# Performance work log

Measured on AMD Instinct MI355X. Metric: run time of the kernel, lower is better.

## Reference

```python
import jax, jax.numpy as jnp
import numpy as np

B, T, I, H = 256, 512, 128, 256


def setup_inputs() -> dict:
    key = jax.random.key(0)
    ks = jax.random.split(key, 12)
    xav = lambda k, shape: jax.random.normal(k, shape, jnp.float32) * jnp.sqrt(2.0 / (shape[0] + shape[1]))
    return {
        'x': jax.random.normal(ks[0], (B, T, I), jnp.float32),
        'weight_xr': xav(ks[1], (H, I)), 'weight_hr': xav(ks[2], (H, H)), 'bias_r': jnp.zeros((H,), jnp.float32),
        'weight_xz': xav(ks[3], (H, I)), 'weight_hz': xav(ks[4], (H, H)), 'bias_z': jnp.zeros((H,), jnp.float32),
        'weight_x': xav(ks[5], (H, I)), 'weight_h': xav(ks[6], (H, H)), 'bias': jnp.zeros((H,), jnp.float32),
        'w1': xav(ks[7], (64, H)), 'b1': jnp.zeros((64,), jnp.float32),
        'w2': xav(ks[8], (10, 64)), 'b2': jnp.zeros((10,), jnp.float32),
    }


def _gru_final(x, weight_xr, weight_hr, bias_r, weight_xz, weight_hz, bias_z,
               weight_x, weight_h, bias):
    # Precompute input projections for all timesteps: [B,T,H] each
    xr = jnp.einsum('bti,hi->bth', x, weight_xr) + bias_r
    xz = jnp.einsum('bti,hi->bth', x, weight_xz) + bias_z
    xn = jnp.einsum('bti,hi->bth', x, weight_x) + bias

    def step(h, inp):
        xr_t, xz_t, xn_t = inp  # each [B,H]
        r = jax.nn.sigmoid(xr_t + h @ weight_hr.T)
        z = jax.nn.sigmoid(xz_t + h @ weight_hz.T)
        ht = jnp.tanh(xn_t + (r * h) @ weight_h.T)
        h_new = z * h + (1.0 - z) * ht
        return h_new, None

    h0 = jnp.zeros((x.shape[0], weight_hr.shape[0]), x.dtype)
    # scan over time: inputs [T,B,H]
    h_final, _ = jax.lax.scan(step, h0, (xr.transpose(1, 0, 2), xz.transpose(1, 0, 2), xn.transpose(1, 0, 2)))
    return h_final


def reference(x, weight_xr, weight_hr, bias_r, weight_xz, weight_hz, bias_z,
              weight_x, weight_h, bias, w1, b1, w2, b2):
    h = _gru_final(x, weight_xr, weight_hr, bias_r, weight_xz, weight_hz, bias_z,
                   weight_x, weight_h, bias)
    h = jax.nn.sigmoid(h)
    h = jax.nn.sigmoid(h @ w1.T + b1)
    return jax.nn.softmax(h @ w2.T + b2, axis=1)
```

## Files before the change

### kernel.cpp

```cpp
#include <hip/hip_runtime.h>


typedef _Float16 half8 __attribute__((ext_vector_type(8)));
typedef float    f32x4 __attribute__((ext_vector_type(4)));

#define BARRIER() asm volatile("s_waitcnt lgkmcnt(0)\n\ts_barrier" ::: "memory")

__device__ __forceinline__ unsigned short f2s(float f) {
    _Float16 h = (_Float16)f; unsigned short s; __builtin_memcpy(&s, &h, 2); return s;
}
__device__ __forceinline__ float s2f(unsigned short s) {
    _Float16 h; __builtin_memcpy(&h, &s, 2); return (float)h;
}
__device__ __forceinline__ float fast_sigmoid(float x) {
    return __builtin_amdgcn_rcpf(1.0f + __builtin_amdgcn_exp2f(-1.4426950408889634f * x));
}
__device__ __forceinline__ float fast_tanh(float x) {
    return 1.0f - 2.0f * __builtin_amdgcn_rcpf(1.0f + __builtin_amdgcn_exp2f(2.885390081777927f * x));
}
__device__ __forceinline__ unsigned int pk2(float lo, float hi) {
    return (unsigned int)f2s(lo) | ((unsigned int)f2s(hi) << 16);
}
__device__ __forceinline__ f32x4 up4(uint2 u) {
    return (f32x4){ s2f((unsigned short)u.x), s2f((unsigned short)(u.x >> 16)),
                    s2f((unsigned short)u.y), s2f((unsigned short)(u.y >> 16)) };
}
union H8U4 { half8 h; uint4 u; };
__device__ __forceinline__ half8 ldg_h8(const unsigned short* p) {
    H8U4 t; t.u = *reinterpret_cast<const uint4*>(p); return t.h;
}
__device__ __forceinline__ half8 pack8(float4 a, float4 b) {
    half8 r;
    r[0] = (_Float16)a.x; r[1] = (_Float16)a.y; r[2] = (_Float16)a.z; r[3] = (_Float16)a.w;
    r[4] = (_Float16)b.x; r[5] = (_Float16)b.y; r[6] = (_Float16)b.z; r[7] = (_Float16)b.w;
    return r;
}

__global__ void pack_w_kernel(const float* __restrict__ whr, const float* __restrict__ whz,
                              const float* __restrict__ wh,  const float* __restrict__ wxr,
                              const float* __restrict__ wxz, const float* __restrict__ wxn,
                              unsigned short* __restrict__ Wall) {
    const int i = blockIdx.x * 256 + threadIdx.x;
    float v;
    if (i < 196608) {
        const int m = i >> 16;
        const int r = i & 65535;
        v = (m == 0 ? whr : (m == 1 ? whz : wh))[r];
    } else {
        const int ii = i - 196608;
        const int m = ii >> 15;
        const int r = ii & 32767;
        v = (m == 0 ? wxr : (m == 1 ? wxz : wxn))[r];
    }
    Wall[i] = f2s(v);
}

__global__ __launch_bounds__(512, 1) void proj_kernel(
    const float* __restrict__ x, const unsigned short* __restrict__ Wxp,
    const float* __restrict__ br, const float* __restrict__ bz, const float* __restrict__ bn,
    unsigned short* __restrict__ P, int t0, int TPB) {
    const int tid = threadIdx.x;
    const int w   = tid >> 6;
    const int lane = tid & 63;
    const int l15 = lane & 15;
    const int lq  = lane >> 4;
    const int btile = blockIdx.x & 15;
    const int tc    = blockIdx.x >> 4;
    const int b0 = btile * 16;

    half8 wf[3][4][2];
#pragma unroll
    for (int g = 0; g < 3; ++g)
#pragma unroll
        for (int kt = 0; kt < 4; ++kt)
#pragma unroll
            for (int ntl = 0; ntl < 2; ++ntl)
                wf[g][kt][ntl] = ldg_h8(Wxp + g * 32768 + (w * 32 + ntl * 16 + l15) * 128 + kt * 32 + 8 * lq);

    const float* bptr[3] = {br, bz, bn};
    float4 bv[3][2];
#pragma unroll
    for (int g = 0; g < 3; ++g)
#pragma unroll
        for (int ntl = 0; ntl < 2; ++ntl)
            bv[g][ntl] = *reinterpret_cast<const float4*>(bptr[g] + (2 * w + ntl) * 16 + 4 * lq);

    for (int i = 0; i < TPB; ++i) {
        const int tl = tc * TPB + i;
        const int t  = t0 + tl;
        half8 xf[4];
#pragma unroll
        for (int kt = 0; kt < 4; ++kt) {
            const float* xp = x + (size_t)(b0 + l15) * 65536 + t * 128 + kt * 32 + 8 * lq;
            float4 f0 = *reinterpret_cast<const float4*>(xp);
            float4 f1 = *reinterpret_cast<const float4*>(xp + 4);
            xf[kt] = pack8(f0, f1);
        }
        unsigned short* Pb = P + (size_t)tl * 196608 + btile * 12288;
#pragma unroll
        for (int g = 0; g < 3; ++g) {
#pragma unroll
            for (int ntl = 0; ntl < 2; ++ntl) {
                f32x4 acc = {0.f, 0.f, 0.f, 0.f};
#pragma unroll
                for (int kt = 0; kt < 4; ++kt)
                    acc = __builtin_amdgcn_mfma_f32_16x16x32_f16(wf[g][kt][ntl], xf[kt], acc, 0, 0, 0);
                uint2 o;
                o.x = pk2(acc[0] + bv[g][ntl].x, acc[1] + bv[g][ntl].y);
                o.y = pk2(acc[2] + bv[g][ntl].z, acc[3] + bv[g][ntl].w);
                *reinterpret_cast<uint2*>(Pb + (2 * w + ntl) * 768 + g * 256 + lane * 4) = o;
            }
        }
    }
}

__global__ __launch_bounds__(512, 1) void rec_kernel(
    const unsigned short* __restrict__ Wp, const unsigned short* __restrict__ P,
    float* __restrict__ h_state, int t0, int Tc) {
    const int tid = threadIdx.x;
    const int w = tid >> 6;
    const int lane = tid & 63;
    const int l15 = lane & 15;
    const int lq = lane >> 4;
    const int btile = blockIdx.x;
    const int b0 = btile * 16;

    __shared__ __align__(16) unsigned short hl[8192];
    char* lds = reinterpret_cast<char*>(hl);

    half8 wr[8][2], wz[8][2], wn[8][2];
#pragma unroll
    for (int kt = 0; kt < 8; ++kt) {
#pragma unroll
        for (int nt = 0; nt < 2; ++nt) {
            const int row = w * 32 + nt * 16 + l15;
            const int co = kt * 32 + 8 * lq;
            wr[kt][nt] = ldg_h8(Wp + row * 256 + co);
            wz[kt][nt] = ldg_h8(Wp + 65536 + row * 256 + co);
            wn[kt][nt] = ldg_h8(Wp + 131072 + row * 256 + co);
        }
    }

    const int b7 = l15 & 7;
    int rdaddr[8];
#pragma unroll
    for (int kt = 0; kt < 8; ++kt)
        rdaddr[kt] = l15 * 512 + (((4 * kt + lq) ^ b7) << 4);
    int waddr[2];
#pragma unroll
    for (int nt = 0; nt < 2; ++nt) {
        const int c = 4 * w + 2 * nt + (lq >> 1);
        waddr[nt] = l15 * 512 + ((c ^ b7) << 4) + 8 * (lq & 1);
    }

    float hreg[2][4];
    if (t0 == 0) {
#pragma unroll
        for (int nt = 0; nt < 2; ++nt)
#pragma unroll
            for (int j = 0; j < 4; ++j) hreg[nt][j] = 0.f;
    } else {
#pragma unroll
        for (int nt = 0; nt < 2; ++nt) {
            float4 v = *reinterpret_cast<const float4*>(
                h_state + (b0 + l15) * 256 + w * 32 + nt * 16 + 4 * lq);
            hreg[nt][0] = v.x; hreg[nt][1] = v.y; hreg[nt][2] = v.z; hreg[nt][3] = v.w;
        }
    }
#pragma unroll
    for (int nt = 0; nt < 2; ++nt) {
        uint2 o;
        o.x = pk2(hreg[nt][0], hreg[nt][1]);
        o.y = pk2(hreg[nt][2], hreg[nt][3]);
        *reinterpret_cast<uint2*>(lds + waddr[nt]) = o;
    }
    BARRIER();

    const unsigned short* Pw = P + btile * 12288 + (2 * w) * 768 + lane * 4;
    uint2 cp[3][2], np[3][2];
#pragma unroll
    for (int g = 0; g < 3; ++g)
#pragma unroll
        for (int nt = 0; nt < 2; ++nt)
            cp[g][nt] = *reinterpret_cast<const uint2*>(Pw + nt * 768 + g * 256);

    for (int tl = 0; tl < Tc; ++tl) {
        const unsigned short* Pn = Pw + (size_t)((tl + 1 < Tc) ? tl + 1 : tl) * 196608;
#pragma unroll
        for (int g = 0; g < 3; ++g)
#pragma unroll
            for (int nt = 0; nt < 2; ++nt)
                np[g][nt] = *reinterpret_cast<const uint2*>(Pn + nt * 768 + g * 256);

        f32x4 aR[2], aZ[2];
        aR[0] = up4(cp[0][0]);
        aR[1] = up4(cp[0][1]);
        aZ[0] = up4(cp[1][0]);
        aZ[1] = up4(cp[1][1]);
#pragma unroll
        for (int kt = 0; kt < 8; ++kt) {
            half8 a = *reinterpret_cast<const half8*>(lds + rdaddr[kt]);
            aR[0] = __builtin_amdgcn_mfma_f32_16x16x32_f16(wr[kt][0], a, aR[0], 0, 0, 0);
            aR[1] = __builtin_amdgcn_mfma_f32_16x16x32_f16(wr[kt][1], a, aR[1], 0, 0, 0);
            aZ[0] = __builtin_amdgcn_mfma_f32_16x16x32_f16(wz[kt][0], a, aZ[0], 0, 0, 0);
            aZ[1] = __builtin_amdgcn_mfma_f32_16x16x32_f16(wz[kt][1], a, aZ[1], 0, 0, 0);
        }
#pragma unroll
        for (int nt = 0; nt < 2; ++nt) {
            const float r0 = fast_sigmoid(aR[nt][0]);
            const float r1 = fast_sigmoid(aR[nt][1]);
            const float r2 = fast_sigmoid(aR[nt][2]);
            const float r3 = fast_sigmoid(aR[nt][3]);
            uint2 o;
            o.x = pk2(r0 * hreg[nt][0], r1 * hreg[nt][1]);
            o.y = pk2(r2 * hreg[nt][2], r3 * hreg[nt][3]);
            *reinterpret_cast<uint2*>(lds + 8192 + waddr[nt]) = o;
        }
        BARRIER();

        float zv[2][4];
#pragma unroll
        for (int nt = 0; nt < 2; ++nt) {
            zv[nt][0] = fast_sigmoid(aZ[nt][0]);
            zv[nt][1] = fast_sigmoid(aZ[nt][1]);
            zv[nt][2] = fast_sigmoid(aZ[nt][2]);
            zv[nt][3] = fast_sigmoid(aZ[nt][3]);
        }
        f32x4 aN[2];
        aN[0] = up4(cp[2][0]);
        aN[1] = up4(cp[2][1]);
#pragma unroll
        for (int kt = 0; kt < 8; ++kt) {
            half8 rf = *reinterpret_cast<const half8*>(lds + 8192 + rdaddr[kt]);
            aN[0] = __builtin_amdgcn_mfma_f32_16x16x32_f16(wn[kt][0], rf, aN[0], 0, 0, 0);
            aN[1] = __builtin_amdgcn_mfma_f32_16x16x32_f16(wn[kt][1], rf, aN[1], 0, 0, 0);
        }
#pragma unroll
        for (int nt = 0; nt < 2; ++nt) {
            const float t0_ = fast_tanh(aN[nt][0]);
            const float t1_ = fast_tanh(aN[nt][1]);
            const float t2_ = fast_tanh(aN[nt][2]);
            const float t3_ = fast_tanh(aN[nt][3]);
            hreg[nt][0] = t0_ + zv[nt][0] * (hreg[nt][0] - t0_);
            hreg[nt][1] = t1_ + zv[nt][1] * (hreg[nt][1] - t1_);
            hreg[nt][2] = t2_ + zv[nt][2] * (hreg[nt][2] - t2_);
            hreg[nt][3] = t3_ + zv[nt][3] * (hreg[nt][3] - t3_);
            uint2 o;
            o.x = pk2(hreg[nt][0], hreg[nt][1]);
            o.y = pk2(hreg[nt][2], hreg[nt][3]);
            *reinterpret_cast<uint2*>(lds + waddr[nt]) = o;
        }
        BARRIER();

#pragma unroll
        for (int g = 0; g < 3; ++g)
#pragma unroll
            for (int nt = 0; nt < 2; ++nt)
                cp[g][nt] = np[g][nt];
    }

#pragma unroll
    for (int nt = 0; nt < 2; ++nt) {
        float4 st;
        st.x = hreg[nt][0]; st.y = hreg[nt][1]; st.z = hreg[nt][2]; st.w = hreg[nt][3];
        *reinterpret_cast<float4*>(h_state + (b0 + l15) * 256 + w * 32 + nt * 16 + 4 * lq) = st;
    }
}

__global__ __launch_bounds__(64) void head_kernel(
    const float* __restrict__ h_state, const float* __restrict__ w1, const float* __restrict__ b1,
    const float* __restrict__ w2, const float* __restrict__ b2, float* __restrict__ out) {
    const int row = blockIdx.x;
    const int lane = threadIdx.x;
    __shared__ float hs[256];
    __shared__ float h2[64];
    __shared__ float lg[10];
    float4 v = *reinterpret_cast<const float4*>(h_state + row * 256 + lane * 4);
    hs[lane * 4 + 0] = fast_sigmoid(v.x);
    hs[lane * 4 + 1] = fast_sigmoid(v.y);
    hs[lane * 4 + 2] = fast_sigmoid(v.z);
    hs[lane * 4 + 3] = fast_sigmoid(v.w);
    __syncthreads();
    float acc = b1[lane];
#pragma unroll 4
    for (int k = 0; k < 256; k += 4) {
        float4 wv = *reinterpret_cast<const float4*>(w1 + lane * 256 + k);
        acc += hs[k] * wv.x + hs[k + 1] * wv.y + hs[k + 2] * wv.z + hs[k + 3] * wv.w;
    }
    h2[lane] = fast_sigmoid(acc);
    __syncthreads();
    if (lane < 10) {
        float a2 = b2[lane];
        for (int k = 0; k < 64; ++k) a2 += h2[k] * w2[lane * 64 + k];
        lg[lane] = a2;
    }
    __syncthreads();
    if (lane < 10) {
        float m = lg[0];
#pragma unroll
        for (int k = 1; k < 10; ++k) m = fmaxf(m, lg[k]);
        float s = 0.f;
#pragma unroll
        for (int k = 0; k < 10; ++k) s += __expf(lg[k] - m);
        out[row * 10 + lane] = __expf(lg[lane] - m) / s;
    }
}

extern "C" void kernel_launch(void* const* d_in, const int* in_sizes, int n_in,
                              void* d_out, int out_size, void* d_ws, size_t ws_size,
                              hipStream_t stream) {
    const float* x   = (const float*)d_in[0];
    const float* wxr = (const float*)d_in[1];
    const float* whr = (const float*)d_in[2];
    const float* br  = (const float*)d_in[3];
    const float* wxz = (const float*)d_in[4];
    const float* whz = (const float*)d_in[5];
    const float* bz  = (const float*)d_in[6];
    const float* wxn = (const float*)d_in[7];
    const float* wh  = (const float*)d_in[8];
    const float* bn  = (const float*)d_in[9];
    const float* w1  = (const float*)d_in[10];
    const float* b1  = (const float*)d_in[11];
    const float* w2  = (const float*)d_in[12];
    const float* b2  = (const float*)d_in[13];
    float* out = (float*)d_out;

    char* ws = (char*)d_ws;
    unsigned short* Wp  = (unsigned short*)ws;
    unsigned short* Wxp = (unsigned short*)(ws + 393216);
    float* h_state = (float*)(ws + 589824);
    unsigned short* P = (unsigned short*)(ws + 851968);
    const size_t avail = (ws_size > 851968) ? ws_size - 851968 : 0;
    int Tc = 512;
    while (Tc > 1 && (size_t)Tc * 393216 > avail) Tc >>= 1;
    const int TPB = Tc < 32 ? Tc : 32;

    pack_w_kernel<<<dim3(1152), 256, 0, stream>>>(whr, whz, wh, wxr, wxz, wxn, Wp);
    for (int t0 = 0; t0 < 512; t0 += Tc) {
        proj_kernel<<<dim3(16 * (Tc / TPB)), 512, 0, stream>>>(x, Wxp, br, bz, bn, P, t0, TPB);
        rec_kernel<<<dim3(16), 512, 0, stream>>>(Wp, P, h_state, t0, Tc);
    }
    head_kernel<<<dim3(256), 64, 0, stream>>>(h_state, w1, b1, w2, b2, out);
}
```

Baseline: 912.6 us.

## Halve recurrence block to 4 waves, each computing 64 hidden columns

The recurrent kernel now launches 256 threads instead of 512, and each wave computes four 16-column tiles of the three gates instead of two. The intent is to cut barrier participants and reuse each LDS read of the hidden state across more MFMAs. In exchange, per-wave register pressure doubles because weights for 64 rows of all three gates are held in registers. There are also fewer waves per SIMD to hide MFMA and transcendental latency on the serial timestep chain.

```diff
diff --git a/kernel.cpp b/kernel.cpp
--- a/kernel.cpp
+++ b/kernel.cpp
@@ -114,7 +114,7 @@
     }
 }
 
-__global__ __launch_bounds__(512, 1) void rec_kernel(
+__global__ __launch_bounds__(256, 1) void rec_kernel(
     const unsigned short* __restrict__ Wp, const unsigned short* __restrict__ P,
     float* __restrict__ h_state, int t0, int Tc) {
     const int tid = threadIdx.x;
@@ -128,16 +128,16 @@
     __shared__ __align__(16) unsigned short hl[8192];
     char* lds = reinterpret_cast<char*>(hl);
 
-    half8 wr[8][2], wz[8][2], wn[8][2];
+    half8 wr[8][4], wz[8][4], wn[8][4];
 #pragma unroll
     for (int kt = 0; kt < 8; ++kt) {
 #pragma unroll
-        for (int nt = 0; nt < 2; ++nt) {
-            const int row = w * 32 + nt * 16 + l15;
+        for (int ntl = 0; ntl < 4; ++ntl) {
+            const int row = w * 64 + ntl * 16 + l15;
             const int co = kt * 32 + 8 * lq;
-            wr[kt][nt] = ldg_h8(Wp + row * 256 + co);
-            wz[kt][nt] = ldg_h8(Wp + 65536 + row * 256 + co);
-            wn[kt][nt] = ldg_h8(Wp + 131072 + row * 256 + co);
+            wr[kt][ntl] = ldg_h8(Wp + row * 256 + co);
+            wz[kt][ntl] = ldg_h8(Wp + 65536 + row * 256 + co);
+            wn[kt][ntl] = ldg_h8(Wp + 131072 + row * 256 + co);
         }
     }
 
@@ -146,124 +146,128 @@
 #pragma unroll
     for (int kt = 0; kt < 8; ++kt)
         rdaddr[kt] = l15 * 512 + (((4 * kt + lq) ^ b7) << 4);
-    int waddr[2];
-#pragma unroll
-    for (int nt = 0; nt < 2; ++nt) {
-        const int c = 4 * w + 2 * nt + (lq >> 1);
-        waddr[nt] = l15 * 512 + ((c ^ b7) << 4) + 8 * (lq & 1);
-    }
-
-    float hreg[2][4];
+    int waddr[4];
+#pragma unroll
+    for (int ntl = 0; ntl < 4; ++ntl) {
+        const int c = 8 * w + 2 * ntl + (lq >> 1);
+        waddr[ntl] = l15 * 512 + ((c ^ b7) << 4) + 8 * (lq & 1);
+    }
+
+    float hreg[4][4];
     if (t0 == 0) {
 #pragma unroll
-        for (int nt = 0; nt < 2; ++nt)
-#pragma unroll
-            for (int j = 0; j < 4; ++j) hreg[nt][j] = 0.f;
+        for (int ntl = 0; ntl < 4; ++ntl)
+#pragma unroll
+            for (int j = 0; j < 4; ++j) hreg[ntl][j] = 0.f;
     } else {
 #pragma unroll
-        for (int nt = 0; nt < 2; ++nt) {
+        for (int ntl = 0; ntl < 4; ++ntl) {
             float4 v = *reinterpret_cast<const float4*>(
-                h_state + (b0 + l15) * 256 + w * 32 + nt * 16 + 4 * lq);
-            hreg[nt][0] = v.x; hreg[nt][1] = v.y; hreg[nt][2] = v.z; hreg[nt][3] = v.w;
-        }
-    }
-#pragma unroll
-    for (int nt = 0; nt < 2; ++nt) {
+                h_state + (b0 + l15) * 256 + w * 64 + ntl * 16 + 4 * lq);
+            hreg[ntl][0] = v.x; hreg[ntl][1] = v.y; hreg[ntl][2] = v.z; hreg[ntl][3] = v.w;
+        }
+    }
+#pragma unroll
+    for (int ntl = 0; ntl < 4; ++ntl) {
         uint2 o;
-        o.x = pk2(hreg[nt][0], hreg[nt][1]);
-        o.y = pk2(hreg[nt][2], hreg[nt][3]);
-        *reinterpret_cast<uint2*>(lds + waddr[nt]) = o;
+        o.x = pk2(hreg[ntl][0], hreg[ntl][1]);
+        o.y = pk2(hreg[ntl][2], hreg[ntl][3]);
+        *reinterpret_cast<uint2*>(lds + waddr[ntl]) = o;
     }
     BARRIER();
 
-    const unsigned short* Pw = P + btile * 12288 + (2 * w) * 768 + lane * 4;
-    uint2 cp[3][2], np[3][2];
+    const unsigned short* Pw = P + btile * 12288 + (4 * w) * 768 + lane * 4;
+    uint2 cp[3][4], np[3][4];
 #pragma unroll
     for (int g = 0; g < 3; ++g)
 #pragma unroll
-        for (int nt = 0; nt < 2; ++nt)
-            cp[g][nt] = *reinterpret_cast<const uint2*>(Pw + nt * 768 + g * 256);
+        for (int ntl = 0; ntl < 4; ++ntl)
+            cp[g][ntl] = *reinterpret_cast<const uint2*>(Pw + ntl * 768 + g * 256);
 
     for (int tl = 0; tl < Tc; ++tl) {
         const unsigned short* Pn = Pw + (size_t)((tl + 1 < Tc) ? tl + 1 : tl) * 196608;
 #pragma unroll
         for (int g = 0; g < 3; ++g)
 #pragma unroll
-            for (int nt = 0; nt < 2; ++nt)
-                np[g][nt] = *reinterpret_cast<const uint2*>(Pn + nt * 768 + g * 256);
-
-        f32x4 aR[2], aZ[2];
-        aR[0] = up4(cp[0][0]);
-        aR[1] = up4(cp[0][1]);
-        aZ[0] = up4(cp[1][0]);
-        aZ[1] = up4(cp[1][1]);
+            for (int ntl = 0; ntl < 4; ++ntl)
+                np[g][ntl] = *reinterpret_cast<const uint2*>(Pn + ntl * 768 + g * 256);
+
+        f32x4 aR[4], aZ[4];
+#pragma unroll
+        for (int ntl = 0; ntl < 4; ++ntl) {
+            aR[ntl] = up4(cp[0][ntl]);
+            aZ[ntl] = up4(cp[1][ntl]);
+        }
 #pragma unroll
         for (int kt = 0; kt < 8; ++kt) {
             half8 a = *reinterpret_cast<const half8*>(lds + rdaddr[kt]);
-            aR[0] = __builtin_amdgcn_mfma_f32_16x16x32_f16(wr[kt][0], a, aR[0], 0, 0, 0);
-            aR[1] = __builtin_amdgcn_mfma_f32_16x16x32_f16(wr[kt][1], a, aR[1], 0, 0, 0);
-            aZ[0] = __builtin_amdgcn_mfma_f32_16x16x32_f16(wz[kt][0], a, aZ[0], 0, 0, 0);
-            aZ[1] = __builtin_amdgcn_mfma_f32_16x16x32_f16(wz[kt][1], a, aZ[1], 0, 0, 0);
-        }
-#pragma unroll
-        for (int nt = 0; nt < 2; ++nt) {
-            const float r0 = fast_sigmoid(aR[nt][0]);
-            const float r1 = fast_sigmoid(aR[nt][1]);
-            const float r2 = fast_sigmoid(aR[nt][2]);
-            const float r3 = fast_sigmoid(aR[nt][3]);
+#pragma unroll
+            for (int ntl = 0; ntl < 4; ++ntl) {
+                aR[ntl] = __builtin_amdgcn_mfma_f32_16x16x32_f16(wr[kt][ntl], a, aR[ntl], 0, 0, 0);
+                aZ[ntl] = __builtin_amdgcn_mfma_f32_16x16x32_f16(wz[kt][ntl], a, aZ[ntl], 0, 0, 0);
+            }
+        }
+#pragma unroll
+        for (int ntl = 0; ntl < 4; ++ntl) {
+            const float r0 = fast_sigmoid(aR[ntl][0]);
+            const float r1 = fast_sigmoid(aR[ntl][1]);
+            const float r2 = fast_sigmoid(aR[ntl][2]);
+            const float r3 = fast_sigmoid(aR[ntl][3]);
             uint2 o;
-            o.x = pk2(r0 * hreg[nt][0], r1 * hreg[nt][1]);
-            o.y = pk2(r2 * hreg[nt][2], r3 * hreg[nt][3]);
-            *reinterpret_cast<uint2*>(lds + 8192 + waddr[nt]) = o;
+            o.x = pk2(r0 * hreg[ntl][0], r1 * hreg[ntl][1]);
+            o.y = pk2(r2 * hreg[ntl][2], r3 * hreg[ntl][3]);
+            *reinterpret_cast<uint2*>(lds + 8192 + waddr[ntl]) = o;
         }
         BARRIER();
 
-        float zv[2][4];
-#pragma unroll
-        for (int nt = 0; nt < 2; ++nt) {
-            zv[nt][0] = fast_sigmoid(aZ[nt][0]);
-            zv[nt][1] = fast_sigmoid(aZ[nt][1]);
-            zv[nt][2] = fast_sigmoid(aZ[nt][2]);
-            zv[nt][3] = fast_sigmoid(aZ[nt][3]);
-        }
-        f32x4 aN[2];
-        aN[0] = up4(cp[2][0]);
-        aN[1] = up4(cp[2][1]);
+        float zv[4][4];
+#pragma unroll
+        for (int ntl = 0; ntl < 4; ++ntl) {
+            zv[ntl][0] = fast_sigmoid(aZ[ntl][0]);
+            zv[ntl][1] = fast_sigmoid(aZ[ntl][1]);
+            zv[ntl][2] = fast_sigmoid(aZ[ntl][2]);
+            zv[ntl][3] = fast_sigmoid(aZ[ntl][3]);
+        }
+        f32x4 aN[4];
+#pragma unroll
+        for (int ntl = 0; ntl < 4; ++ntl)
+            aN[ntl] = up4(cp[2][ntl]);
 #pragma unroll
         for (int kt = 0; kt < 8; ++kt) {
             half8 rf = *reinterpret_cast<const half8*>(lds + 8192 + rdaddr[kt]);
-            aN[0] = __builtin_amdgcn_mfma_f32_16x16x32_f16(wn[kt][0], rf, aN[0], 0, 0, 0);
-            aN[1] = __builtin_amdgcn_mfma_f32_16x16x32_f16(wn[kt][1], rf, aN[1], 0, 0, 0);
-        }
-#pragma unroll
-        for (int nt = 0; nt < 2; ++nt) {
-            const float t0_ = fast_tanh(aN[nt][0]);
-            const float t1_ = fast_tanh(aN[nt][1]);
-            const float t2_ = fast_tanh(aN[nt][2]);
-            const float t3_ = fast_tanh(aN[nt][3]);
-            hreg[nt][0] = t0_ + zv[nt][0] * (hreg[nt][0] - t0_);
-            hreg[nt][1] = t1_ + zv[nt][1] * (hreg[nt][1] - t1_);
-            hreg[nt][2] = t2_ + zv[nt][2] * (hreg[nt][2] - t2_);
-            hreg[nt][3] = t3_ + zv[nt][3] * (hreg[nt][3] - t3_);
+#pragma unroll
+            for (int ntl = 0; ntl < 4; ++ntl)
+                aN[ntl] = __builtin_amdgcn_mfma_f32_16x16x32_f16(wn[kt][ntl], rf, aN[ntl], 0, 0, 0);
+        }
+#pragma unroll
+        for (int ntl = 0; ntl < 4; ++ntl) {
+            const float t0_ = fast_tanh(aN[ntl][0]);
+            const float t1_ = fast_tanh(aN[ntl][1]);
+            const float t2_ = fast_tanh(aN[ntl][2]);
+            const float t3_ = fast_tanh(aN[ntl][3]);
+            hreg[ntl][0] = t0_ + zv[ntl][0] * (hreg[ntl][0] - t0_);
+            hreg[ntl][1] = t1_ + zv[ntl][1] * (hreg[ntl][1] - t1_);
+            hreg[ntl][2] = t2_ + zv[ntl][2] * (hreg[ntl][2] - t2_);
+            hreg[ntl][3] = t3_ + zv[ntl][3] * (hreg[ntl][3] - t3_);
             uint2 o;
-            o.x = pk2(hreg[nt][0], hreg[nt][1]);
-            o.y = pk2(hreg[nt][2], hreg[nt][3]);
-            *reinterpret_cast<uint2*>(lds + waddr[nt]) = o;
+            o.x = pk2(hreg[ntl][0], hreg[ntl][1]);
+            o.y = pk2(hreg[ntl][2], hreg[ntl][3]);
+            *reinterpret_cast<uint2*>(lds + waddr[ntl]) = o;
         }
         BARRIER();
 
 #pragma unroll
         for (int g = 0; g < 3; ++g)
 #pragma unroll
-            for (int nt = 0; nt < 2; ++nt)
-                cp[g][nt] = np[g][nt];
-    }
-
-#pragma unroll
-    for (int nt = 0; nt < 2; ++nt) {
+            for (int ntl = 0; ntl < 4; ++ntl)
+                cp[g][ntl] = np[g][ntl];
+    }
+
+#pragma unroll
+    for (int ntl = 0; ntl < 4; ++ntl) {
         float4 st;
-        st.x = hreg[nt][0]; st.y = hreg[nt][1]; st.z = hreg[nt][2]; st.w = hreg[nt][3];
-        *reinterpret_cast<float4*>(h_state + (b0 + l15) * 256 + w * 32 + nt * 16 + 4 * lq) = st;
+        st.x = hreg[ntl][0]; st.y = hreg[ntl][1]; st.z = hreg[ntl][2]; st.w = hreg[ntl][3];
+        *reinterpret_cast<float4*>(h_state + (b0 + l15) * 256 + w * 64 + ntl * 16 + 4 * lq) = st;
     }
 }
 
@@ -338,7 +342,7 @@
     pack_w_kernel<<<dim3(1152), 256, 0, stream>>>(whr, whz, wh, wxr, wxz, wxn, Wp);
     for (int t0 = 0; t0 < 512; t0 += Tc) {
         proj_kernel<<<dim3(16 * (Tc / TPB)), 512, 0, stream>>>(x, Wxp, br, bz, bn, P, t0, TPB);
-        rec_kernel<<<dim3(16), 512, 0, stream>>>(Wp, P, h_state, t0, Tc);
+        rec_kernel<<<dim3(16), 256, 0, stream>>>(Wp, P, h_state, t0, Tc);
     }
     head_kernel<<<dim3(256), 64, 0, stream>>>(h_state, w1, b1, w2, b2, out);
 }
```

After: 1.203 ms. 31.8% more time.

## Fuse projection and recurrence into one kernel with flag-based producer/consumer overlap

Applied to the files above, without the earlier changes.

Merges the input-projection and recurrent kernels into one launch. 16 blocks run the recurrence while the remaining 112 blocks compute projection chunks and signal completion through per-chunk atomic flags. Recurrence blocks spin-wait on the flags for the current and next chunk. The projection GEMM can then overlap the serial recurrence instead of running entirely before it. The cost is a memset per launch, spin-waits, and reliance on all 128 blocks being resident at once to avoid deadlock.

```diff
diff --git a/kernel.cpp b/kernel.cpp
--- a/kernel.cpp
+++ b/kernel.cpp
@@ -55,78 +55,84 @@
     Wall[i] = f2s(v);
 }
 
-__global__ __launch_bounds__(512, 1) void proj_kernel(
-    const float* __restrict__ x, const unsigned short* __restrict__ Wxp,
+__global__ __launch_bounds__(512, 1) void fused_kernel(
+    const float* __restrict__ x, const unsigned short* __restrict__ Wp,
+    const unsigned short* __restrict__ Wxp,
     const float* __restrict__ br, const float* __restrict__ bz, const float* __restrict__ bn,
-    unsigned short* __restrict__ P, int t0, int TPB) {
-    const int tid = threadIdx.x;
-    const int w   = tid >> 6;
-    const int lane = tid & 63;
-    const int l15 = lane & 15;
-    const int lq  = lane >> 4;
-    const int btile = blockIdx.x & 15;
-    const int tc    = blockIdx.x >> 4;
-    const int b0 = btile * 16;
-
-    half8 wf[3][4][2];
-#pragma unroll
-    for (int g = 0; g < 3; ++g)
-#pragma unroll
-        for (int kt = 0; kt < 4; ++kt)
-#pragma unroll
-            for (int ntl = 0; ntl < 2; ++ntl)
-                wf[g][kt][ntl] = ldg_h8(Wxp + g * 32768 + (w * 32 + ntl * 16 + l15) * 128 + kt * 32 + 8 * lq);
-
-    const float* bptr[3] = {br, bz, bn};
-    float4 bv[3][2];
-#pragma unroll
-    for (int g = 0; g < 3; ++g)
-#pragma unroll
-        for (int ntl = 0; ntl < 2; ++ntl)
-            bv[g][ntl] = *reinterpret_cast<const float4*>(bptr[g] + (2 * w + ntl) * 16 + 4 * lq);
-
-    for (int i = 0; i < TPB; ++i) {
-        const int tl = tc * TPB + i;
-        const int t  = t0 + tl;
-        half8 xf[4];
-#pragma unroll
-        for (int kt = 0; kt < 4; ++kt) {
-            const float* xp = x + (size_t)(b0 + l15) * 65536 + t * 128 + kt * 32 + 8 * lq;
-            float4 f0 = *reinterpret_cast<const float4*>(xp);
-            float4 f1 = *reinterpret_cast<const float4*>(xp + 4);
-            xf[kt] = pack8(f0, f1);
-        }
-        unsigned short* Pb = P + (size_t)tl * 196608 + btile * 12288;
-#pragma unroll
-        for (int g = 0; g < 3; ++g) {
-#pragma unroll
-            for (int ntl = 0; ntl < 2; ++ntl) {
-                f32x4 acc = {0.f, 0.f, 0.f, 0.f};
-#pragma unroll
-                for (int kt = 0; kt < 4; ++kt)
-                    acc = __builtin_amdgcn_mfma_f32_16x16x32_f16(wf[g][kt][ntl], xf[kt], acc, 0, 0, 0);
-                uint2 o;
-                o.x = pk2(acc[0] + bv[g][ntl].x, acc[1] + bv[g][ntl].y);
-                o.y = pk2(acc[2] + bv[g][ntl].z, acc[3] + bv[g][ntl].w);
-                *reinterpret_cast<uint2*>(Pb + (2 * w + ntl) * 768 + g * 256 + lane * 4) = o;
-            }
-        }
-    }
-}
-
-__global__ __launch_bounds__(512, 1) void rec_kernel(
-    const unsigned short* __restrict__ Wp, const unsigned short* __restrict__ P,
-    float* __restrict__ h_state, int t0, int Tc) {
+    unsigned short* __restrict__ P, float* __restrict__ h_state, int* __restrict__ flags,
+    int t0, int Tc, int CH, int NC) {
     const int tid = threadIdx.x;
     const int w = tid >> 6;
     const int lane = tid & 63;
     const int l15 = lane & 15;
     const int lq = lane >> 4;
+
+    __shared__ __align__(16) unsigned short hl[8192];
+    char* lds = reinterpret_cast<char*>(hl);
+
+    if (blockIdx.x >= 16) {
+        const int pb = blockIdx.x - 16;
+        const int NPROJ = (int)gridDim.x - 16;
+
+        half8 wf[3][4][2];
+#pragma unroll
+        for (int g = 0; g < 3; ++g)
+#pragma unroll
+            for (int kt = 0; kt < 4; ++kt)
+#pragma unroll
+                for (int ntl = 0; ntl < 2; ++ntl)
+                    wf[g][kt][ntl] = ldg_h8(Wxp + g * 32768 + (w * 32 + ntl * 16 + l15) * 128 + kt * 32 + 8 * lq);
+
+        const float* bptr[3] = {br, bz, bn};
+        float4 bv[3][2];
+#pragma unroll
+        for (int g = 0; g < 3; ++g)
+#pragma unroll
+            for (int ntl = 0; ntl < 2; ++ntl)
+                bv[g][ntl] = *reinterpret_cast<const float4*>(bptr[g] + (2 * w + ntl) * 16 + 4 * lq);
+
+        const int NI = NC * 16;
+        for (int it = pb; it < NI; it += NPROJ) {
+            const int c  = it >> 4;
+            const int bt = it & 15;
+            const int b0 = bt * 16;
+            for (int i = 0; i < CH; ++i) {
+                const int tl = c * CH + i;
+                const int t  = t0 + tl;
+                half8 xf[4];
+#pragma unroll
+                for (int kt = 0; kt < 4; ++kt) {
+                    const float* xp = x + (size_t)(b0 + l15) * 65536 + t * 128 + kt * 32 + 8 * lq;
+                    float4 f0 = *reinterpret_cast<const float4*>(xp);
+                    float4 f1 = *reinterpret_cast<const float4*>(xp + 4);
+                    xf[kt] = pack8(f0, f1);
+                }
+                unsigned short* Pb = P + (size_t)tl * 196608 + bt * 12288;
+#pragma unroll
+                for (int g = 0; g < 3; ++g) {
+#pragma unroll
+                    for (int ntl = 0; ntl < 2; ++ntl) {
+                        f32x4 acc = {0.f, 0.f, 0.f, 0.f};
+#pragma unroll
+                        for (int kt = 0; kt < 4; ++kt)
+                            acc = __builtin_amdgcn_mfma_f32_16x16x32_f16(wf[g][kt][ntl], xf[kt], acc, 0, 0, 0);
+                        uint2 o;
+                        o.x = pk2(acc[0] + bv[g][ntl].x, acc[1] + bv[g][ntl].y);
+                        o.y = pk2(acc[2] + bv[g][ntl].z, acc[3] + bv[g][ntl].w);
+                        *reinterpret_cast<uint2*>(Pb + (2 * w + ntl) * 768 + g * 256 + lane * 4) = o;
+                    }
+                }
+            }
+            __threadfence();
+            __syncthreads();
+            if (tid == 0)
+                __hip_atomic_fetch_add(&flags[c], 1, __ATOMIC_RELEASE, __HIP_MEMORY_SCOPE_AGENT);
+        }
+        return;
+    }
+
     const int btile = blockIdx.x;
     const int b0 = btile * 16;
-
-    __shared__ __align__(16) unsigned short hl[8192];
-    char* lds = reinterpret_cast<char*>(hl);
 
     half8 wr[8][2], wz[8][2], wn[8][2];
 #pragma unroll
@@ -178,85 +184,103 @@
 
     const unsigned short* Pw = P + btile * 12288 + (2 * w) * 768 + lane * 4;
     uint2 cp[3][2], np[3][2];
-#pragma unroll
-    for (int g = 0; g < 3; ++g)
-#pragma unroll
-        for (int nt = 0; nt < 2; ++nt)
-            cp[g][nt] = *reinterpret_cast<const uint2*>(Pw + nt * 768 + g * 256);
-
-    for (int tl = 0; tl < Tc; ++tl) {
-        const unsigned short* Pn = Pw + (size_t)((tl + 1 < Tc) ? tl + 1 : tl) * 196608;
-#pragma unroll
-        for (int g = 0; g < 3; ++g)
-#pragma unroll
-            for (int nt = 0; nt < 2; ++nt)
-                np[g][nt] = *reinterpret_cast<const uint2*>(Pn + nt * 768 + g * 256);
-
-        f32x4 aR[2], aZ[2];
-        aR[0] = up4(cp[0][0]);
-        aR[1] = up4(cp[0][1]);
-        aZ[0] = up4(cp[1][0]);
-        aZ[1] = up4(cp[1][1]);
-#pragma unroll
-        for (int kt = 0; kt < 8; ++kt) {
-            half8 a = *reinterpret_cast<const half8*>(lds + rdaddr[kt]);
-            aR[0] = __builtin_amdgcn_mfma_f32_16x16x32_f16(wr[kt][0], a, aR[0], 0, 0, 0);
-            aR[1] = __builtin_amdgcn_mfma_f32_16x16x32_f16(wr[kt][1], a, aR[1], 0, 0, 0);
-            aZ[0] = __builtin_amdgcn_mfma_f32_16x16x32_f16(wz[kt][0], a, aZ[0], 0, 0, 0);
-            aZ[1] = __builtin_amdgcn_mfma_f32_16x16x32_f16(wz[kt][1], a, aZ[1], 0, 0, 0);
-        }
-#pragma unroll
-        for (int nt = 0; nt < 2; ++nt) {
-            const float r0 = fast_sigmoid(aR[nt][0]);
-            const float r1 = fast_sigmoid(aR[nt][1]);
-            const float r2 = fast_sigmoid(aR[nt][2]);
-            const float r3 = fast_sigmoid(aR[nt][3]);
-            uint2 o;
-            o.x = pk2(r0 * hreg[nt][0], r1 * hreg[nt][1]);
-            o.y = pk2(r2 * hreg[nt][2], r3 * hreg[nt][3]);
-            *reinterpret_cast<uint2*>(lds + 8192 + waddr[nt]) = o;
-        }
-        BARRIER();
-
-        float zv[2][4];
-#pragma unroll
-        for (int nt = 0; nt < 2; ++nt) {
-            zv[nt][0] = fast_sigmoid(aZ[nt][0]);
-            zv[nt][1] = fast_sigmoid(aZ[nt][1]);
-            zv[nt][2] = fast_sigmoid(aZ[nt][2]);
-            zv[nt][3] = fast_sigmoid(aZ[nt][3]);
-        }
-        f32x4 aN[2];
-        aN[0] = up4(cp[2][0]);
-        aN[1] = up4(cp[2][1]);
-#pragma unroll
-        for (int kt = 0; kt < 8; ++kt) {
-            half8 rf = *reinterpret_cast<const half8*>(lds + 8192 + rdaddr[kt]);
-            aN[0] = __builtin_amdgcn_mfma_f32_16x16x32_f16(wn[kt][0], rf, aN[0], 0, 0, 0);
-            aN[1] = __builtin_amdgcn_mfma_f32_16x16x32_f16(wn[kt][1], rf, aN[1], 0, 0, 0);
-        }
-#pragma unroll
-        for (int nt = 0; nt < 2; ++nt) {
-            const float t0_ = fast_tanh(aN[nt][0]);
-            const float t1_ = fast_tanh(aN[nt][1]);
-            const float t2_ = fast_tanh(aN[nt][2]);
-            const float t3_ = fast_tanh(aN[nt][3]);
-            hreg[nt][0] = t0_ + zv[nt][0] * (hreg[nt][0] - t0_);
-            hreg[nt][1] = t1_ + zv[nt][1] * (hreg[nt][1] - t1_);
-            hreg[nt][2] = t2_ + zv[nt][2] * (hreg[nt][2] - t2_);
-            hreg[nt][3] = t3_ + zv[nt][3] * (hreg[nt][3] - t3_);
-            uint2 o;
-            o.x = pk2(hreg[nt][0], hreg[nt][1]);
-            o.y = pk2(hreg[nt][2], hreg[nt][3]);
-            *reinterpret_cast<uint2*>(lds + waddr[nt]) = o;
-        }
-        BARRIER();
-
-#pragma unroll
-        for (int g = 0; g < 3; ++g)
-#pragma unroll
-            for (int nt = 0; nt < 2; ++nt)
-                cp[g][nt] = np[g][nt];
+
+    for (int c = 0; c < NC; ++c) {
+        const int cw = (c + 1 < NC) ? c + 1 : c;
+        if (tid == 0) {
+            while (__hip_atomic_load(&flags[c],  __ATOMIC_ACQUIRE, __HIP_MEMORY_SCOPE_AGENT) < 16 ||
+                   __hip_atomic_load(&flags[cw], __ATOMIC_ACQUIRE, __HIP_MEMORY_SCOPE_AGENT) < 16)
+                __builtin_amdgcn_s_sleep(16);
+        }
+        __syncthreads();
+        {
+            int f = __hip_atomic_load(&flags[c], __ATOMIC_ACQUIRE, __HIP_MEMORY_SCOPE_AGENT);
+            asm volatile("" :: "v"(f) : "memory");
+        }
+        if (c == 0) {
+#pragma unroll
+            for (int g = 0; g < 3; ++g)
+#pragma unroll
+                for (int nt = 0; nt < 2; ++nt)
+                    cp[g][nt] = *reinterpret_cast<const uint2*>(Pw + nt * 768 + g * 256);
+        }
+
+        const int tbeg = c * CH;
+        for (int i = 0; i < CH; ++i) {
+            const int tl = tbeg + i;
+            const unsigned short* Pn = Pw + (size_t)((tl + 1 < Tc) ? tl + 1 : tl) * 196608;
+#pragma unroll
+            for (int g = 0; g < 3; ++g)
+#pragma unroll
+                for (int nt = 0; nt < 2; ++nt)
+                    np[g][nt] = *reinterpret_cast<const uint2*>(Pn + nt * 768 + g * 256);
+
+            f32x4 aR[2], aZ[2];
+            aR[0] = up4(cp[0][0]);
+            aR[1] = up4(cp[0][1]);
+            aZ[0] = up4(cp[1][0]);
+            aZ[1] = up4(cp[1][1]);
+#pragma unroll
+            for (int kt = 0; kt < 8; ++kt) {
+                half8 a = *reinterpret_cast<const half8*>(lds + rdaddr[kt]);
+                aR[0] = __builtin_amdgcn_mfma_f32_16x16x32_f16(wr[kt][0], a, aR[0], 0, 0, 0);
+                aR[1] = __builtin_amdgcn_mfma_f32_16x16x32_f16(wr[kt][1], a, aR[1], 0, 0, 0);
+                aZ[0] = __builtin_amdgcn_mfma_f32_16x16x32_f16(wz[kt][0], a, aZ[0], 0, 0, 0);
+                aZ[1] = __builtin_amdgcn_mfma_f32_16x16x32_f16(wz[kt][1], a, aZ[1], 0, 0, 0);
+            }
+#pragma unroll
+            for (int nt = 0; nt < 2; ++nt) {
+                const float r0 = fast_sigmoid(aR[nt][0]);
+                const float r1 = fast_sigmoid(aR[nt][1]);
+                const float r2 = fast_sigmoid(aR[nt][2]);
+                const float r3 = fast_sigmoid(aR[nt][3]);
+                uint2 o;
+                o.x = pk2(r0 * hreg[nt][0], r1 * hreg[nt][1]);
+                o.y = pk2(r2 * hreg[nt][2], r3 * hreg[nt][3]);
+                *reinterpret_cast<uint2*>(lds + 8192 + waddr[nt]) = o;
+            }
+            BARRIER();
+
+            float zv[2][4];
+#pragma unroll
+            for (int nt = 0; nt < 2; ++nt) {
+                zv[nt][0] = fast_sigmoid(aZ[nt][0]);
+                zv[nt][1] = fast_sigmoid(aZ[nt][1]);
+                zv[nt][2] = fast_sigmoid(aZ[nt][2]);
+                zv[nt][3] = fast_sigmoid(aZ[nt][3]);
+            }
+            f32x4 aN[2];
+            aN[0] = up4(cp[2][0]);
+            aN[1] = up4(cp[2][1]);
+#pragma unroll
+            for (int kt = 0; kt < 8; ++kt) {
+                half8 rf = *reinterpret_cast<const half8*>(lds + 8192 + rdaddr[kt]);
+                aN[0] = __builtin_amdgcn_mfma_f32_16x16x32_f16(wn[kt][0], rf, aN[0], 0, 0, 0);
+                aN[1] = __builtin_amdgcn_mfma_f32_16x16x32_f16(wn[kt][1], rf, aN[1], 0, 0, 0);
+            }
+#pragma unroll
+            for (int nt = 0; nt < 2; ++nt) {
+                const float t0_ = fast_tanh(aN[nt][0]);
+                const float t1_ = fast_tanh(aN[nt][1]);
+                const float t2_ = fast_tanh(aN[nt][2]);
+                const float t3_ = fast_tanh(aN[nt][3]);
+                hreg[nt][0] = t0_ + zv[nt][0] * (hreg[nt][0] - t0_);
+                hreg[nt][1] = t1_ + zv[nt][1] * (hreg[nt][1] - t1_);
+                hreg[nt][2] = t2_ + zv[nt][2] * (hreg[nt][2] - t2_);
+                hreg[nt][3] = t3_ + zv[nt][3] * (hreg[nt][3] - t3_);
+                uint2 o;
+                o.x = pk2(hreg[nt][0], hreg[nt][1]);
+                o.y = pk2(hreg[nt][2], hreg[nt][3]);
+                *reinterpret_cast<uint2*>(lds + waddr[nt]) = o;
+            }
+            BARRIER();
+
+#pragma unroll
+            for (int g = 0; g < 3; ++g)
+#pragma unroll
+                for (int nt = 0; nt < 2; ++nt)
+                    cp[g][nt] = np[g][nt];
+        }
     }
 
 #pragma unroll
@@ -330,15 +354,17 @@
     unsigned short* Wxp = (unsigned short*)(ws + 393216);
     float* h_state = (float*)(ws + 589824);
     unsigned short* P = (unsigned short*)(ws + 851968);
-    const size_t avail = (ws_size > 851968) ? ws_size - 851968 : 0;
     int Tc = 512;
-    while (Tc > 1 && (size_t)Tc * 393216 > avail) Tc >>= 1;
-    const int TPB = Tc < 32 ? Tc : 32;
+    while (Tc > 1 && 851968 + (size_t)Tc * 393216 + 256 > ws_size) Tc >>= 1;
+    const int CH = Tc < 32 ? Tc : 32;
+    const int NC = Tc / CH;
+    int* flags = (int*)(ws + 851968 + (size_t)Tc * 393216);
 
     pack_w_kernel<<<dim3(1152), 256, 0, stream>>>(whr, whz, wh, wxr, wxz, wxn, Wp);
     for (int t0 = 0; t0 < 512; t0 += Tc) {
-        proj_kernel<<<dim3(16 * (Tc / TPB)), 512, 0, stream>>>(x, Wxp, br, bz, bn, P, t0, TPB);
-        rec_kernel<<<dim3(16), 512, 0, stream>>>(Wp, P, h_state, t0, Tc);
+        hipMemsetAsync(flags, 0, NC * sizeof(int), stream);
+        fused_kernel<<<dim3(128), 512, 0, stream>>>(x, Wp, Wxp, br, bz, bn, P, h_state,
+                                                    flags, t0, Tc, CH, NC);
     }
     head_kernel<<<dim3(256), 64, 0, stream>>>(h_state, w1, b1, w2, b2, out);
 }
```

After: 1.000 ms. 1.1x slower.

## Drop weight pack kernel, fuse head into recurrence, unroll steps by two

Applied to the files above, without the earlier changes.

Removes the separate fp16 weight-packing kernel; the projection and recurrent kernels now load fp32 weights directly and convert them in registers. The classifier head (sigmoid, two small dense layers, softmax) is folded into the last recurrent kernel launch using LDS, which removes a launch and a round trip through h_state. The time loop is unrolled by two with ping-pong prefetch buffers so the register copy of the next step's projections goes away. This saves two kernel launches at the cost of doing the fp32 weight loads and conversions inside each kernel, and of running the head on only 16 blocks.

```diff
diff --git a/kernel.cpp b/kernel.cpp
--- a/kernel.cpp
+++ b/kernel.cpp
@@ -24,10 +24,6 @@
 __device__ __forceinline__ f32x4 up4(uint2 u) {
     return (f32x4){ s2f((unsigned short)u.x), s2f((unsigned short)(u.x >> 16)),
                     s2f((unsigned short)u.y), s2f((unsigned short)(u.y >> 16)) };
-}
-union H8U4 { half8 h; uint4 u; };
-__device__ __forceinline__ half8 ldg_h8(const unsigned short* p) {
-    H8U4 t; t.u = *reinterpret_cast<const uint4*>(p); return t.h;
 }
 __device__ __forceinline__ half8 pack8(float4 a, float4 b) {
     half8 r;
@@ -35,28 +31,15 @@
     r[4] = (_Float16)b.x; r[5] = (_Float16)b.y; r[6] = (_Float16)b.z; r[7] = (_Float16)b.w;
     return r;
 }
-
-__global__ void pack_w_kernel(const float* __restrict__ whr, const float* __restrict__ whz,
-                              const float* __restrict__ wh,  const float* __restrict__ wxr,
-                              const float* __restrict__ wxz, const float* __restrict__ wxn,
-                              unsigned short* __restrict__ Wall) {
-    const int i = blockIdx.x * 256 + threadIdx.x;
-    float v;
-    if (i < 196608) {
-        const int m = i >> 16;
-        const int r = i & 65535;
-        v = (m == 0 ? whr : (m == 1 ? whz : wh))[r];
-    } else {
-        const int ii = i - 196608;
-        const int m = ii >> 15;
-        const int r = ii & 32767;
-        v = (m == 0 ? wxr : (m == 1 ? wxz : wxn))[r];
-    }
-    Wall[i] = f2s(v);
+__device__ __forceinline__ half8 ldg8_f32(const float* p) {
+    float4 a = *reinterpret_cast<const float4*>(p);
+    float4 b = *reinterpret_cast<const float4*>(p + 4);
+    return pack8(a, b);
 }
 
 __global__ __launch_bounds__(512, 1) void proj_kernel(
-    const float* __restrict__ x, const unsigned short* __restrict__ Wxp,
+    const float* __restrict__ x,
+    const float* __restrict__ wxr, const float* __restrict__ wxz, const float* __restrict__ wxn,
     const float* __restrict__ br, const float* __restrict__ bz, const float* __restrict__ bn,
     unsigned short* __restrict__ P, int t0, int TPB) {
     const int tid = threadIdx.x;
@@ -68,6 +51,7 @@
     const int tc    = blockIdx.x >> 4;
     const int b0 = btile * 16;
 
+    const float* wptr[3] = {wxr, wxz, wxn};
     half8 wf[3][4][2];
 #pragma unroll
     for (int g = 0; g < 3; ++g)
@@ -75,7 +59,7 @@
         for (int kt = 0; kt < 4; ++kt)
 #pragma unroll
             for (int ntl = 0; ntl < 2; ++ntl)
-                wf[g][kt][ntl] = ldg_h8(Wxp + g * 32768 + (w * 32 + ntl * 16 + l15) * 128 + kt * 32 + 8 * lq);
+                wf[g][kt][ntl] = ldg8_f32(wptr[g] + (w * 32 + ntl * 16 + l15) * 128 + kt * 32 + 8 * lq);
 
     const float* bptr[3] = {br, bz, bn};
     float4 bv[3][2];
@@ -90,12 +74,8 @@
         const int t  = t0 + tl;
         half8 xf[4];
 #pragma unroll
-        for (int kt = 0; kt < 4; ++kt) {
-            const float* xp = x + (size_t)(b0 + l15) * 65536 + t * 128 + kt * 32 + 8 * lq;
-            float4 f0 = *reinterpret_cast<const float4*>(xp);
-            float4 f1 = *reinterpret_cast<const float4*>(xp + 4);
-            xf[kt] = pack8(f0, f1);
-        }
+        for (int kt = 0; kt < 4; ++kt)
+            xf[kt] = ldg8_f32(x + (size_t)(b0 + l15) * 65536 + t * 128 + kt * 32 + 8 * lq);
         unsigned short* Pb = P + (size_t)tl * 196608 + btile * 12288;
 #pragma unroll
         for (int g = 0; g < 3; ++g) {
@@ -115,8 +95,10 @@
 }
 
 __global__ __launch_bounds__(512, 1) void rec_kernel(
-    const unsigned short* __restrict__ Wp, const unsigned short* __restrict__ P,
-    float* __restrict__ h_state, int t0, int Tc) {
+    const float* __restrict__ whr, const float* __restrict__ whz, const float* __restrict__ wh,
+    const unsigned short* __restrict__ P, float* __restrict__ h_state, int t0, int Tc, int last,
+    const float* __restrict__ w1, const float* __restrict__ b1,
+    const float* __restrict__ w2, const float* __restrict__ b2, float* __restrict__ out) {
     const int tid = threadIdx.x;
     const int w = tid >> 6;
     const int lane = tid & 63;
@@ -135,9 +117,9 @@
         for (int nt = 0; nt < 2; ++nt) {
             const int row = w * 32 + nt * 16 + l15;
             const int co = kt * 32 + 8 * lq;
-            wr[kt][nt] = ldg_h8(Wp + row * 256 + co);
-            wz[kt][nt] = ldg_h8(Wp + 65536 + row * 256 + co);
-            wn[kt][nt] = ldg_h8(Wp + 131072 + row * 256 + co);
+            wr[kt][nt] = ldg8_f32(whr + row * 256 + co);
+            wz[kt][nt] = ldg8_f32(whz + row * 256 + co);
+            wn[kt][nt] = ldg8_f32(wh  + row * 256 + co);
         }
     }
 
@@ -177,15 +159,14 @@
     BARRIER();
 
     const unsigned short* Pw = P + btile * 12288 + (2 * w) * 768 + lane * 4;
-    uint2 cp[3][2], np[3][2];
+    uint2 cpA[3][2], cpB[3][2];
 #pragma unroll
     for (int g = 0; g < 3; ++g)
 #pragma unroll
         for (int nt = 0; nt < 2; ++nt)
-            cp[g][nt] = *reinterpret_cast<const uint2*>(Pw + nt * 768 + g * 256);
-
-    for (int tl = 0; tl < Tc; ++tl) {
-        const unsigned short* Pn = Pw + (size_t)((tl + 1 < Tc) ? tl + 1 : tl) * 196608;
+            cpA[g][nt] = *reinterpret_cast<const uint2*>(Pw + nt * 768 + g * 256);
+
+    auto STEP = [&](uint2 (&cp)[3][2], uint2 (&np)[3][2], const unsigned short* Pn) {
 #pragma unroll
         for (int g = 0; g < 3; ++g)
 #pragma unroll
@@ -251,12 +232,15 @@
             *reinterpret_cast<uint2*>(lds + waddr[nt]) = o;
         }
         BARRIER();
-
-#pragma unroll
-        for (int g = 0; g < 3; ++g)
-#pragma unroll
-            for (int nt = 0; nt < 2; ++nt)
-                cp[g][nt] = np[g][nt];
+    };
+
+    for (int tl = 0; tl < Tc; tl += 2) {
+        const unsigned short* Pn1 = Pw + (size_t)((tl + 1 < Tc) ? tl + 1 : Tc - 1) * 196608;
+        STEP(cpA, cpB, Pn1);
+        if (tl + 1 < Tc) {
+            const unsigned short* Pn2 = Pw + (size_t)((tl + 2 < Tc) ? tl + 2 : Tc - 1) * 196608;
+            STEP(cpB, cpA, Pn2);
+        }
     }
 
 #pragma unroll
@@ -265,44 +249,66 @@
         st.x = hreg[nt][0]; st.y = hreg[nt][1]; st.z = hreg[nt][2]; st.w = hreg[nt][3];
         *reinterpret_cast<float4*>(h_state + (b0 + l15) * 256 + w * 32 + nt * 16 + 4 * lq) = st;
     }
-}
-
-__global__ __launch_bounds__(64) void head_kernel(
-    const float* __restrict__ h_state, const float* __restrict__ w1, const float* __restrict__ b1,
-    const float* __restrict__ w2, const float* __restrict__ b2, float* __restrict__ out) {
-    const int row = blockIdx.x;
-    const int lane = threadIdx.x;
-    __shared__ float hs[256];
-    __shared__ float h2[64];
-    __shared__ float lg[10];
-    float4 v = *reinterpret_cast<const float4*>(h_state + row * 256 + lane * 4);
-    hs[lane * 4 + 0] = fast_sigmoid(v.x);
-    hs[lane * 4 + 1] = fast_sigmoid(v.y);
-    hs[lane * 4 + 2] = fast_sigmoid(v.z);
-    hs[lane * 4 + 3] = fast_sigmoid(v.w);
-    __syncthreads();
-    float acc = b1[lane];
+
+    if (!last) return;
+
+    float* hf32 = reinterpret_cast<float*>(hl);
+    BARRIER();
+#pragma unroll
+    for (int nt = 0; nt < 2; ++nt) {
+        float4 sv;
+        sv.x = fast_sigmoid(hreg[nt][0]);
+        sv.y = fast_sigmoid(hreg[nt][1]);
+        sv.z = fast_sigmoid(hreg[nt][2]);
+        sv.w = fast_sigmoid(hreg[nt][3]);
+        *reinterpret_cast<float4*>(&hf32[l15 * 256 + w * 32 + nt * 16 + 4 * lq]) = sv;
+    }
+    BARRIER();
+
+    float h2v[2];
+#pragma unroll
+    for (int rr = 0; rr < 2; ++rr) {
+        const int r = 2 * w + rr;
+        float acc = b1[lane];
 #pragma unroll 4
-    for (int k = 0; k < 256; k += 4) {
-        float4 wv = *reinterpret_cast<const float4*>(w1 + lane * 256 + k);
-        acc += hs[k] * wv.x + hs[k + 1] * wv.y + hs[k + 2] * wv.z + hs[k + 3] * wv.w;
-    }
-    h2[lane] = fast_sigmoid(acc);
-    __syncthreads();
+        for (int k = 0; k < 256; k += 4) {
+            float4 hv = *reinterpret_cast<const float4*>(&hf32[r * 256 + k]);
+            float4 wv = *reinterpret_cast<const float4*>(w1 + lane * 256 + k);
+            acc += hv.x * wv.x + hv.y * wv.y + hv.z * wv.z + hv.w * wv.w;
+        }
+        h2v[rr] = fast_sigmoid(acc);
+    }
+    BARRIER();
+    float* h2s = hf32;
+#pragma unroll
+    for (int rr = 0; rr < 2; ++rr)
+        h2s[(2 * w + rr) * 64 + lane] = h2v[rr];
+    BARRIER();
+
+    float* lg = hf32 + 1024;
     if (lane < 10) {
-        float a2 = b2[lane];
-        for (int k = 0; k < 64; ++k) a2 += h2[k] * w2[lane * 64 + k];
-        lg[lane] = a2;
-    }
-    __syncthreads();
+#pragma unroll
+        for (int rr = 0; rr < 2; ++rr) {
+            const int r = 2 * w + rr;
+            float a2 = b2[lane];
+#pragma unroll 8
+            for (int k = 0; k < 64; ++k) a2 += h2s[r * 64 + k] * w2[lane * 64 + k];
+            lg[r * 16 + lane] = a2;
+        }
+    }
+    BARRIER();
     if (lane < 10) {
-        float m = lg[0];
-#pragma unroll
-        for (int k = 1; k < 10; ++k) m = fmaxf(m, lg[k]);
-        float s = 0.f;
-#pragma unroll
-        for (int k = 0; k < 10; ++k) s += __expf(lg[k] - m);
-        out[row * 10 + lane] = __expf(lg[lane] - m) / s;
+#pragma unroll
+        for (int rr = 0; rr < 2; ++rr) {
+            const int r = 2 * w + rr;
+            float m = lg[r * 16 + 0];
+#pragma unroll
+            for (int k = 1; k < 10; ++k) m = fmaxf(m, lg[r * 16 + k]);
+            float s = 0.f;
+#pragma unroll
+            for (int k = 0; k < 10; ++k) s += __expf(lg[r * 16 + k] - m);
+            out[(b0 + r) * 10 + lane] = __expf(lg[r * 16 + lane] - m) / s;
+        }
     }
 }
 
@@ -326,8 +332,6 @@
     float* out = (float*)d_out;
 
     char* ws = (char*)d_ws;
-    unsigned short* Wp  = (unsigned short*)ws;
-    unsigned short* Wxp = (unsigned short*)(ws + 393216);
     float* h_state = (float*)(ws + 589824);
     unsigned short* P = (unsigned short*)(ws + 851968);
     const size_t avail = (ws_size > 851968) ? ws_size - 851968 : 0;
@@ -335,10 +339,11 @@
     while (Tc > 1 && (size_t)Tc * 393216 > avail) Tc >>= 1;
     const int TPB = Tc < 32 ? Tc : 32;
 
-    pack_w_kernel<<<dim3(1152), 256, 0, stream>>>(whr, whz, wh, wxr, wxz, wxn, Wp);
     for (int t0 = 0; t0 < 512; t0 += Tc) {
-        proj_kernel<<<dim3(16 * (Tc / TPB)), 512, 0, stream>>>(x, Wxp, br, bz, bn, P, t0, TPB);
-        rec_kernel<<<dim3(16), 512, 0, stream>>>(Wp, P, h_state, t0, Tc);
-    }
-    head_kernel<<<dim3(256), 64, 0, stream>>>(h_state, w1, b1, w2, b2, out);
-}
+        const int last = (t0 + Tc >= 512) ? 1 : 0;
+        proj_kernel<<<dim3(16 * (Tc / TPB)), 512, 0, stream>>>(x, wxr, wxz, wxn,
+                                                               br, bz, bn, P, t0, TPB);
+        rec_kernel<<<dim3(16), 512, 0, stream>>>(whr, whz, wh, P, h_state, t0, Tc, last,
+                                                 w1, b1, w2, b2, out);
+    }
+}
```

Result: slower. 1.131 ms (+23.9%).
